# Kernel tuning notes

Measured on AMD Instinct MI355X. Metric: run time of the kernel, lower is better.

The kernel has to match this reference:

```python
import jax, jax.numpy as jnp
import numpy as np

K = 5        # up_kernel
SIG = 2      # scale_factor
PAD = K // 2

def _conv(x, w, b, pad):
    y = jax.lax.conv_general_dilated(
        x, w, window_strides=(1, 1), padding=[(pad, pad), (pad, pad)],
        dimension_numbers=('NCHW', 'OIHW', 'NCHW'))
    return y + b[None, :, None, None]

def setup_inputs() -> dict:
    key = jax.random.key(0)
    k1, k2, k3 = jax.random.split(key, 3)
    n, c, h, w = 4, 256, 64, 64
    comp_c = 64
    enc_out = K * K * 1 * SIG * SIG  # 100
    x = jax.random.normal(k1, (n, c, h, w), dtype=jnp.float32)
    w_comp = jax.random.normal(k2, (comp_c, c, 1, 1), dtype=jnp.float32) * (1.0 / np.sqrt(c))
    b_comp = jnp.zeros((comp_c,), dtype=jnp.float32)
    w_enc = jax.random.normal(k3, (enc_out, comp_c, 3, 3), dtype=jnp.float32) * 0.001
    b_enc = jnp.zeros((enc_out,), dtype=jnp.float32)
    return {"x": x, "w_comp": w_comp, "b_comp": b_comp, "w_enc": w_enc, "b_enc": b_enc}

def reference(x, w_comp, b_comp, w_enc, b_enc):
    n, c, h, w = x.shape
    # 1) channel compressor (1x1 conv) + content encoder (3x3 conv, pad 1)
    compressed = _conv(x, w_comp, b_comp, pad=0)
    mask = _conv(compressed, w_enc, b_enc, pad=1)        # [n, K*K*SIG*SIG, h, w]
    # 2) kernel_normalizer: pixel_shuffle(sigma) then softmax over K*K
    # torch pixel_shuffle channel layout: (K*K, SIG, SIG)
    mask = mask.reshape(n, K * K, SIG, SIG, h, w)
    mask = jax.nn.softmax(mask, axis=1)                   # softmax over kernel taps
    # 3) CARAFE reassembly: gather KxK window around each low-res source pixel
    xp = jnp.pad(x, ((0, 0), (0, 0), (PAD, PAD), (PAD, PAD)))
    # patches: [n, c, K*K, h, w]  (zero-padded borders)
    patches = jnp.stack(
        [xp[:, :, di:di + h, dj:dj + w] for di in range(K) for dj in range(K)],
        axis=2)
    # out[n,c,h*SIG+i, w*SIG+j] = sum_k patches[n,c,k,h,w] * mask[n,k,i,j,h,w]
    out = jnp.einsum('nkijhw,nckhw->nchiwj', mask, patches)
    return out.reshape(n, c, h * SIG, w * SIG)
```

## Files before the change

kernel.cpp:

```cpp
#include <hip/hip_runtime.h>

#define HW      4096
#define W_DIM   64
#define C_IN    256
#define NK      25
#define NQ      112

typedef __bf16 bf16x4 __attribute__((ext_vector_type(4)));
typedef __bf16 bf16x8 __attribute__((ext_vector_type(8)));
typedef float  f32x4  __attribute__((ext_vector_type(4)));
typedef float  f32x2  __attribute__((ext_vector_type(2)));

static __device__ __forceinline__ unsigned short f2bf(float f) {
    unsigned x = __float_as_uint(f);
    return (unsigned short)((x + 0x7fffu + ((x >> 16) & 1u)) >> 16);
}
static __device__ __forceinline__ float bflo2f(unsigned u) { return __uint_as_float(u << 16); }
static __device__ __forceinline__ float bfhi2f(unsigned u) { return __uint_as_float(u & 0xffff0000u); }

__global__ __launch_bounds__(256) void k_prep(const float* __restrict__ wenc,
                                              const float* __restrict__ wcomp,
                                              unsigned short* __restrict__ wtb,
                                              unsigned short* __restrict__ wct) {
    int idx = blockIdx.x * 256 + threadIdx.x;
    if (idx < 64512) {
        int c = idx & 63;
        int t2 = idx >> 6;
        int kq = t2 % NQ;
        int tap = t2 / NQ;
        float v = (kq < 100) ? wenc[(kq * 64 + c) * 9 + tap] : 0.0f;
        wtb[idx] = f2bf(v);
    } else if (idx < 80896) {
        int j = idx - 64512;
        wct[j] = f2bf(wcomp[j]);
    }
}

__global__ __launch_bounds__(256) void k_compress(const float* __restrict__ x,
        const unsigned short* __restrict__ wct, const float* __restrict__ bcomp,
        unsigned short* __restrict__ comp) {
    __shared__ unsigned short As[64 * 260];
    __shared__ unsigned short Bs[64 * 260];
    __shared__ float sbc[64];
    int n = blockIdx.y, p0 = blockIdx.x * 64;
    int tid = threadIdx.x, wv = tid >> 6, lane = tid & 63;
    int l15 = lane & 15, l4 = lane >> 4;
    if (tid < 64) sbc[tid] = bcomp[tid];

    const float* xp = x + (size_t)n * C_IN * HW + p0;
#pragma unroll
    for (int s = 0; s < 32; ++s) {
        int cp = s * 4 + wv;
        float a = xp[(size_t)(2 * cp) * HW + lane];
        float b = xp[(size_t)(2 * cp + 1) * HW + lane];
        unsigned pk = (unsigned)f2bf(a) | ((unsigned)f2bf(b) << 16);
        *(unsigned*)(As + lane * 260 + cp * 2) = pk;
    }
    const unsigned* wsrc = (const unsigned*)wct;
#pragma unroll
    for (int s = 0; s < 32; ++s) {
        int slot = s * 256 + tid;
        int cc = slot >> 7, c2 = slot & 127;
        *(unsigned*)(Bs + cc * 260 + c2 * 2) = wsrc[cc * 128 + c2];
    }
    __syncthreads();

    f32x4 acc[4];
#pragma unroll
    for (int nt = 0; nt < 4; ++nt) acc[nt] = (f32x4){0.f, 0.f, 0.f, 0.f};
#pragma unroll
    for (int ck = 0; ck < 8; ++ck) {
        int ko = ck * 32 + l4 * 8;
        bf16x4 alo = *(const bf16x4*)(As + (wv * 16 + l15) * 260 + ko);
        bf16x4 ahi = *(const bf16x4*)(As + (wv * 16 + l15) * 260 + ko + 4);
        bf16x8 af = __builtin_shufflevector(alo, ahi, 0, 1, 2, 3, 4, 5, 6, 7);
#pragma unroll
        for (int nt = 0; nt < 4; ++nt) {
            bf16x4 blo = *(const bf16x4*)(Bs + (nt * 16 + l15) * 260 + ko);
            bf16x4 bhi = *(const bf16x4*)(Bs + (nt * 16 + l15) * 260 + ko + 4);
            bf16x8 bfr = __builtin_shufflevector(blo, bhi, 0, 1, 2, 3, 4, 5, 6, 7);
            acc[nt] = __builtin_amdgcn_mfma_f32_16x16x32_bf16(af, bfr, acc[nt], 0, 0, 0);
        }
    }
    unsigned short* op = comp + ((size_t)n * HW + p0 + wv * 16 + l4 * 4) * 64;
#pragma unroll
    for (int reg = 0; reg < 4; ++reg)
#pragma unroll
        for (int nt = 0; nt < 4; ++nt) {
            int cc = nt * 16 + l15;
            op[(size_t)reg * 64 + cc] = f2bf(acc[nt][reg] + sbc[cc]);
        }
}

#define CREC    136
#define SB0     13600
#define BSTRIDE 15232
#define EPI_PAD 116
__global__ __launch_bounds__(256) void k_enc(
        const unsigned short* __restrict__ comp,
        const unsigned short* __restrict__ wtb,
        const float* __restrict__ benc,
        unsigned short* __restrict__ mask) {
    __shared__ __align__(16) unsigned char smem[SB0 + 2 * BSTRIDE];
    __shared__ float sbias[NQ];
    int n = blockIdx.y, tile = blockIdx.x;
    int h0 = (tile >> 3) * 8, w0 = (tile & 7) * 8;
    int tid = threadIdx.x, wv = tid >> 6, lane = tid & 63;
    int l15 = lane & 15, l4 = lane >> 4;
    if (tid < NQ) sbias[tid] = (tid < 100) ? benc[tid] : 0.0f;

    const uint4* csrc = (const uint4*)(comp + (size_t)n * HW * 64);
#pragma unroll
    for (int pass = 0; pass < 4; ++pass) {
        int s = pass * 256 + tid;
        if (s < 800) {
            int px = s >> 3, j = s & 7;
            int gh = h0 + px / 10 - 1, gw = w0 + px % 10 - 1;
            uint4 v = make_uint4(0u, 0u, 0u, 0u);
            if ((unsigned)gh < 64u && (unsigned)gw < 64u)
                v = csrc[(size_t)(gh * 64 + gw) * 8 + j];
            *(uint2*)(smem + px * CREC + j * 16)     = make_uint2(v.x, v.y);
            *(uint2*)(smem + px * CREC + j * 16 + 8) = make_uint2(v.z, v.w);
        }
    }
    {
        const uint4* bs = (const uint4*)wtb;
#pragma unroll
        for (int pass = 0; pass < 4; ++pass) {
            int s = pass * 256 + tid;
            if (s < 896) {
                uint4 v = bs[s];
                int kq = s >> 3, j = s & 7;
                *(uint2*)(smem + SB0 + kq * CREC + j * 16)     = make_uint2(v.x, v.y);
                *(uint2*)(smem + SB0 + kq * CREC + j * 16 + 8) = make_uint2(v.z, v.w);
            }
        }
    }
    uint4 pre[4];
    {
        const uint4* bs = (const uint4*)(wtb + (size_t)1 * NQ * 64);
#pragma unroll
        for (int pass = 0; pass < 4; ++pass) {
            int s = pass * 256 + tid;
            if (s < 896) pre[pass] = bs[s];
        }
    }

    f32x4 acc[7];
#pragma unroll
    for (int nt = 0; nt < 7; ++nt) acc[nt] = (f32x4){0.f, 0.f, 0.f, 0.f};
    int r_t = 2 * wv + (l15 >> 3), cl = l15 & 7;

    for (int tap = 0; tap < 9; ++tap) {
        __syncthreads();
        if (tap < 8) {
            unsigned char* nbuf = smem + SB0 + ((tap + 1) & 1) * BSTRIDE;
#pragma unroll
            for (int pass = 0; pass < 4; ++pass) {
                int s = pass * 256 + tid;
                if (s < 896) {
                    int kq = s >> 3, j = s & 7;
                    *(uint2*)(nbuf + kq * CREC + j * 16)     = make_uint2(pre[pass].x, pre[pass].y);
                    *(uint2*)(nbuf + kq * CREC + j * 16 + 8) = make_uint2(pre[pass].z, pre[pass].w);
                }
            }
            if (tap < 7) {
                const uint4* bs = (const uint4*)(wtb + (size_t)(tap + 2) * NQ * 64);
#pragma unroll
                for (int pass = 0; pass < 4; ++pass) {
                    int s = pass * 256 + tid;
                    if (s < 896) pre[pass] = bs[s];
                }
            }
        }
        int ti = tap / 3, tj = tap % 3;
        int apx = (r_t + ti) * 10 + cl + tj;
        const unsigned char* cbuf = smem + SB0 + (tap & 1) * BSTRIDE;
#pragma unroll
        for (int ck = 0; ck < 2; ++ck) {
            int ko = ck * 64 + l4 * 16;
            bf16x4 alo = *(const bf16x4*)(smem + apx * CREC + ko);
            bf16x4 ahi = *(const bf16x4*)(smem + apx * CREC + ko + 8);
            bf16x8 af = __builtin_shufflevector(alo, ahi, 0, 1, 2, 3, 4, 5, 6, 7);
#pragma unroll
            for (int nt = 0; nt < 7; ++nt) {
                bf16x4 blo = *(const bf16x4*)(cbuf + (nt * 16 + l15) * CREC + ko);
                bf16x4 bhi = *(const bf16x4*)(cbuf + (nt * 16 + l15) * CREC + ko + 8);
                bf16x8 bfr = __builtin_shufflevector(blo, bhi, 0, 1, 2, 3, 4, 5, 6, 7);
                acc[nt] = __builtin_amdgcn_mfma_f32_16x16x32_bf16(af, bfr, acc[nt], 0, 0, 0);
            }
        }
    }
    __syncthreads();

    float* smE = (float*)(smem + SB0) + (size_t)wv * 16 * EPI_PAD;
    unsigned short* maskn = mask + (size_t)n * HW * 100;
#pragma unroll
    for (int nt = 0; nt < 7; ++nt) {
        f32x4 v = acc[nt];
#pragma unroll
        for (int reg = 0; reg < 4; ++reg)
            smE[(l4 * 4 + reg) * EPI_PAD + nt * 16 + l15] = v[reg];
    }
    {
        int spx = lane >> 2, q = lane & 3;
        float* row = smE + spx * EPI_PAD;
        float v[NK], mx = -1e30f;
#pragma unroll
        for (int k = 0; k < NK; ++k) {
            v[k] = row[4 * k + q] + sbias[4 * k + q];
            mx = fmaxf(mx, v[k]);
        }
        float ssum = 0.f;
#pragma unroll
        for (int k = 0; k < NK; ++k) { v[k] = __expf(v[k] - mx); ssum += v[k]; }
        float inv = 1.0f / ssum;
#pragma unroll
        for (int k = 0; k < NK; ++k) row[4 * k + q] = v[k] * inv;
    }
#pragma unroll
    for (int i = 0; i < 7; ++i) {
        int idx = i * 64 + lane;
        if (idx < 400) {
            int spx = idx / 25, f4 = idx % 25;
            int rr = 2 * wv + (spx >> 3), cc2 = spx & 7;
            size_t p = (size_t)(h0 + rr) * 64 + (w0 + cc2);
            const float* sp = smE + spx * EPI_PAD + f4 * 4;
            unsigned u0 = (unsigned)f2bf(sp[0]) | ((unsigned)f2bf(sp[1]) << 16);
            unsigned u1 = (unsigned)f2bf(sp[2]) | ((unsigned)f2bf(sp[3]) << 16);
            *(uint2*)(maskn + p * 100 + f4 * 4) = make_uint2(u0, u1);
        }
    }
}

#define XSTR2 20
#define MSTR2 108
__global__ __launch_bounds__(256, 6) void k_reassemble(const float* __restrict__ x,
        const unsigned short* __restrict__ mask, float* __restrict__ out) {
    __shared__ __align__(16) float xs[144 * XSTR2];
    __shared__ __align__(16) unsigned short ms[64 * MSTR2];
    int flat = blockIdx.x;
    int nf = (flat & 7) * 512 + (flat >> 3);
    int tile = nf & 63, cg = (nf >> 6) & 15, n = nf >> 10;
    int h0 = (tile >> 3) * 8, w0 = (tile & 7) * 8;
    int tid = threadIdx.x;

    const float* xb = x + ((size_t)n * C_IN + cg * 16) * HW;
#pragma unroll
    for (int i = 0; i < 5; ++i) {
        int s = i * 256 + tid;
        if (s < 1152) {
            int c = s / 72, rem = s % 72;
            int r = rem / 6, j = rem % 6;
            int gh = h0 - 2 + r, gw = w0 - 2 + j * 2;
            float2 v = make_float2(0.f, 0.f);
            if ((unsigned)gh < 64u && (unsigned)gw < 64u)
                v = *(const float2*)(xb + (size_t)c * HW + gh * W_DIM + gw);
            int px = r * 12 + j * 2;
            xs[px * XSTR2 + c]       = v.x;
            xs[(px + 1) * XSTR2 + c] = v.y;
        }
    }
    const unsigned short* mp = mask + (size_t)n * HW * 100;
#pragma unroll
    for (int i = 0; i < 7; ++i) {
        int s = i * 256 + tid;
        if (s < 1600) {
            int px = s / 25, q = s % 25;
            int gp = (h0 + (px >> 3)) * W_DIM + w0 + (px & 7);
            *(uint2*)(ms + px * MSTR2 + q * 4) =
                *(const uint2*)(mp + (size_t)gp * 100 + q * 4);
        }
    }
    __syncthreads();

    int px = tid & 63, w = tid >> 6;
    int wx = px & 7, hy = px >> 3;
    f32x4 acc0 = {0.f, 0.f, 0.f, 0.f}, acc1 = {0.f, 0.f, 0.f, 0.f};
    f32x4 acc2 = {0.f, 0.f, 0.f, 0.f}, acc3 = {0.f, 0.f, 0.f, 0.f};
    const unsigned short* mrow = ms + px * MSTR2;
#pragma unroll
    for (int di = 0; di < 5; ++di)
#pragma unroll
        for (int dj = 0; dj < 5; ++dj) {
            int t = di * 5 + dj;
            uint2 mw = *(const uint2*)(mrow + t * 4);
            f32x4 xv = *(const f32x4*)(xs + ((hy + di) * 12 + wx + dj) * XSTR2 + w * 4);
            acc0 += xv * bflo2f(mw.x);
            acc1 += xv * bfhi2f(mw.x);
            acc2 += xv * bflo2f(mw.y);
            acc3 += xv * bfhi2f(mw.y);
        }
#pragma unroll
    for (int u = 0; u < 4; ++u) {
        float* ob = out + (((size_t)n * C_IN + cg * 16 + w * 4 + u) * 128 + 2 * (h0 + hy)) * 128
                        + 2 * (w0 + wx);
        *(float2*)(ob)       = make_float2(acc0[u], acc1[u]);
        *(float2*)(ob + 128) = make_float2(acc2[u], acc3[u]);
    }
}

extern "C" void kernel_launch(void* const* d_in, const int* in_sizes, int n_in,
                              void* d_out, int out_size, void* d_ws, size_t ws_size,
                              hipStream_t stream) {
    const float* x      = (const float*)d_in[0];
    const float* w_comp = (const float*)d_in[1];
    const float* b_comp = (const float*)d_in[2];
    const float* w_enc  = (const float*)d_in[3];
    const float* b_enc  = (const float*)d_in[4];
    float* out = (float*)d_out;
    unsigned char* ws = (unsigned char*)d_ws;

    unsigned short* comp  = (unsigned short*)(ws);
    unsigned short* wtb   = (unsigned short*)(ws + 2097152);
    unsigned short* wct   = (unsigned short*)(ws + 2226176);
    unsigned short* maskp = (unsigned short*)(ws + 2258944);

    hipLaunchKernelGGL(k_prep,       dim3(316),      dim3(256), 0, stream,
                       w_enc, w_comp, wtb, wct);
    hipLaunchKernelGGL(k_compress,   dim3(64, 4),    dim3(256), 0, stream,
                       x, wct, b_comp, comp);
    hipLaunchKernelGGL(k_enc,        dim3(64, 4),    dim3(256), 0, stream,
                       comp, wtb, b_enc, maskp);
    hipLaunchKernelGGL(k_reassemble, dim3(4096),     dim3(256), 0, stream,
                       x, maskp, out);
}
```

Measured before the change: 121.3 us.

## Spread compress and encoder GEMMs over more waves and smaller tiles

The compress kernel now runs 1024 threads per block, so each of the 16 waves computes one 16x16 output tile instead of four waves each computing four. The encoder kernel halves its spatial tile to 4x8 pixels and doubles the grid. Its four waves split the seven output-channel tiles between two row groups, and the softmax and store epilogue now runs on a shared block-wide staging buffer. The aim is more parallelism and occupancy on small grids (256 blocks) to hide latency. The cost is more barriers, a larger halo overhead, and redundant weight staging per block.

```diff
diff --git a/kernel.cpp b/kernel.cpp
--- a/kernel.cpp
+++ b/kernel.cpp
@@ -36,7 +36,7 @@
     }
 }
 
-__global__ __launch_bounds__(256) void k_compress(const float* __restrict__ x,
+__global__ __launch_bounds__(1024) void k_compress(const float* __restrict__ x,
         const unsigned short* __restrict__ wct, const float* __restrict__ bcomp,
         unsigned short* __restrict__ comp) {
     __shared__ unsigned short As[64 * 260];
@@ -49,8 +49,8 @@
 
     const float* xp = x + (size_t)n * C_IN * HW + p0;
 #pragma unroll
-    for (int s = 0; s < 32; ++s) {
-        int cp = s * 4 + wv;
+    for (int s = 0; s < 8; ++s) {
+        int cp = s * 16 + wv;
         float a = xp[(size_t)(2 * cp) * HW + lane];
         float b = xp[(size_t)(2 * cp + 1) * HW + lane];
         unsigned pk = (unsigned)f2bf(a) | ((unsigned)f2bf(b) << 16);
@@ -58,42 +58,36 @@
     }
     const unsigned* wsrc = (const unsigned*)wct;
 #pragma unroll
-    for (int s = 0; s < 32; ++s) {
-        int slot = s * 256 + tid;
+    for (int s = 0; s < 8; ++s) {
+        int slot = s * 1024 + tid;
         int cc = slot >> 7, c2 = slot & 127;
         *(unsigned*)(Bs + cc * 260 + c2 * 2) = wsrc[cc * 128 + c2];
     }
     __syncthreads();
 
-    f32x4 acc[4];
-#pragma unroll
-    for (int nt = 0; nt < 4; ++nt) acc[nt] = (f32x4){0.f, 0.f, 0.f, 0.f};
+    int mt = wv >> 2, nt = wv & 3;
+    f32x4 acc = (f32x4){0.f, 0.f, 0.f, 0.f};
 #pragma unroll
     for (int ck = 0; ck < 8; ++ck) {
         int ko = ck * 32 + l4 * 8;
-        bf16x4 alo = *(const bf16x4*)(As + (wv * 16 + l15) * 260 + ko);
-        bf16x4 ahi = *(const bf16x4*)(As + (wv * 16 + l15) * 260 + ko + 4);
+        bf16x4 alo = *(const bf16x4*)(As + (mt * 16 + l15) * 260 + ko);
+        bf16x4 ahi = *(const bf16x4*)(As + (mt * 16 + l15) * 260 + ko + 4);
         bf16x8 af = __builtin_shufflevector(alo, ahi, 0, 1, 2, 3, 4, 5, 6, 7);
-#pragma unroll
-        for (int nt = 0; nt < 4; ++nt) {
-            bf16x4 blo = *(const bf16x4*)(Bs + (nt * 16 + l15) * 260 + ko);
-            bf16x4 bhi = *(const bf16x4*)(Bs + (nt * 16 + l15) * 260 + ko + 4);
-            bf16x8 bfr = __builtin_shufflevector(blo, bhi, 0, 1, 2, 3, 4, 5, 6, 7);
-            acc[nt] = __builtin_amdgcn_mfma_f32_16x16x32_bf16(af, bfr, acc[nt], 0, 0, 0);
-        }
-    }
-    unsigned short* op = comp + ((size_t)n * HW + p0 + wv * 16 + l4 * 4) * 64;
-#pragma unroll
-    for (int reg = 0; reg < 4; ++reg)
-#pragma unroll
-        for (int nt = 0; nt < 4; ++nt) {
-            int cc = nt * 16 + l15;
-            op[(size_t)reg * 64 + cc] = f2bf(acc[nt][reg] + sbc[cc]);
-        }
+        bf16x4 blo = *(const bf16x4*)(Bs + (nt * 16 + l15) * 260 + ko);
+        bf16x4 bhi = *(const bf16x4*)(Bs + (nt * 16 + l15) * 260 + ko + 4);
+        bf16x8 bfr = __builtin_shufflevector(blo, bhi, 0, 1, 2, 3, 4, 5, 6, 7);
+        acc = __builtin_amdgcn_mfma_f32_16x16x32_bf16(af, bfr, acc, 0, 0, 0);
+    }
+    unsigned short* op = comp + ((size_t)n * HW + p0 + mt * 16 + l4 * 4) * 64 + nt * 16;
+#pragma unroll
+    for (int reg = 0; reg < 4; ++reg) {
+        int cc = nt * 16 + l15;
+        op[(size_t)reg * 64 + l15] = f2bf(acc[reg] + sbc[cc]);
+    }
 }
 
 #define CREC    136
-#define SB0     13600
+#define SB0E    8160
 #define BSTRIDE 15232
 #define EPI_PAD 116
 __global__ __launch_bounds__(256) void k_enc(
@@ -101,19 +95,19 @@
         const unsigned short* __restrict__ wtb,
         const float* __restrict__ benc,
         unsigned short* __restrict__ mask) {
-    __shared__ __align__(16) unsigned char smem[SB0 + 2 * BSTRIDE];
+    __shared__ __align__(16) unsigned char smem[SB0E + 2 * BSTRIDE];
     __shared__ float sbias[NQ];
     int n = blockIdx.y, tile = blockIdx.x;
-    int h0 = (tile >> 3) * 8, w0 = (tile & 7) * 8;
+    int h0 = (tile >> 3) * 4, w0 = (tile & 7) * 8;
     int tid = threadIdx.x, wv = tid >> 6, lane = tid & 63;
     int l15 = lane & 15, l4 = lane >> 4;
     if (tid < NQ) sbias[tid] = (tid < 100) ? benc[tid] : 0.0f;
 
     const uint4* csrc = (const uint4*)(comp + (size_t)n * HW * 64);
 #pragma unroll
-    for (int pass = 0; pass < 4; ++pass) {
+    for (int pass = 0; pass < 2; ++pass) {
         int s = pass * 256 + tid;
-        if (s < 800) {
+        if (s < 480) {
             int px = s >> 3, j = s & 7;
             int gh = h0 + px / 10 - 1, gw = w0 + px % 10 - 1;
             uint4 v = make_uint4(0u, 0u, 0u, 0u);
@@ -131,8 +125,8 @@
             if (s < 896) {
                 uint4 v = bs[s];
                 int kq = s >> 3, j = s & 7;
-                *(uint2*)(smem + SB0 + kq * CREC + j * 16)     = make_uint2(v.x, v.y);
-                *(uint2*)(smem + SB0 + kq * CREC + j * 16 + 8) = make_uint2(v.z, v.w);
+                *(uint2*)(smem + SB0E + kq * CREC + j * 16)     = make_uint2(v.x, v.y);
+                *(uint2*)(smem + SB0E + kq * CREC + j * 16 + 8) = make_uint2(v.z, v.w);
             }
         }
     }
@@ -146,15 +140,16 @@
         }
     }
 
-    f32x4 acc[7];
-#pragma unroll
-    for (int nt = 0; nt < 7; ++nt) acc[nt] = (f32x4){0.f, 0.f, 0.f, 0.f};
-    int r_t = 2 * wv + (l15 >> 3), cl = l15 & 7;
+    f32x4 acc[4];
+#pragma unroll
+    for (int k = 0; k < 4; ++k) acc[k] = (f32x4){0.f, 0.f, 0.f, 0.f};
+    int mt = wv & 1, ng = wv >> 1;
+    int r_t = 2 * mt + (l15 >> 3), cl = l15 & 7;
 
     for (int tap = 0; tap < 9; ++tap) {
         __syncthreads();
         if (tap < 8) {
-            unsigned char* nbuf = smem + SB0 + ((tap + 1) & 1) * BSTRIDE;
+            unsigned char* nbuf = smem + SB0E + ((tap + 1) & 1) * BSTRIDE;
 #pragma unroll
             for (int pass = 0; pass < 4; ++pass) {
                 int s = pass * 256 + tid;
@@ -175,7 +170,7 @@
         }
         int ti = tap / 3, tj = tap % 3;
         int apx = (r_t + ti) * 10 + cl + tj;
-        const unsigned char* cbuf = smem + SB0 + (tap & 1) * BSTRIDE;
+        const unsigned char* cbuf = smem + SB0E + (tap & 1) * BSTRIDE;
 #pragma unroll
         for (int ck = 0; ck < 2; ++ck) {
             int ko = ck * 64 + l4 * 16;
@@ -183,27 +178,34 @@
             bf16x4 ahi = *(const bf16x4*)(smem + apx * CREC + ko + 8);
             bf16x8 af = __builtin_shufflevector(alo, ahi, 0, 1, 2, 3, 4, 5, 6, 7);
 #pragma unroll
-            for (int nt = 0; nt < 7; ++nt) {
-                bf16x4 blo = *(const bf16x4*)(cbuf + (nt * 16 + l15) * CREC + ko);
-                bf16x4 bhi = *(const bf16x4*)(cbuf + (nt * 16 + l15) * CREC + ko + 8);
-                bf16x8 bfr = __builtin_shufflevector(blo, bhi, 0, 1, 2, 3, 4, 5, 6, 7);
-                acc[nt] = __builtin_amdgcn_mfma_f32_16x16x32_bf16(af, bfr, acc[nt], 0, 0, 0);
+            for (int k = 0; k < 4; ++k) {
+                int nt = ng + 2 * k;
+                if (nt < 7) {
+                    bf16x4 blo = *(const bf16x4*)(cbuf + (nt * 16 + l15) * CREC + ko);
+                    bf16x4 bhi = *(const bf16x4*)(cbuf + (nt * 16 + l15) * CREC + ko + 8);
+                    bf16x8 bfr = __builtin_shufflevector(blo, bhi, 0, 1, 2, 3, 4, 5, 6, 7);
+                    acc[k] = __builtin_amdgcn_mfma_f32_16x16x32_bf16(af, bfr, acc[k], 0, 0, 0);
+                }
             }
         }
     }
     __syncthreads();
 
-    float* smE = (float*)(smem + SB0) + (size_t)wv * 16 * EPI_PAD;
+    float* smE = (float*)(smem + SB0E);
     unsigned short* maskn = mask + (size_t)n * HW * 100;
 #pragma unroll
-    for (int nt = 0; nt < 7; ++nt) {
-        f32x4 v = acc[nt];
-#pragma unroll
-        for (int reg = 0; reg < 4; ++reg)
-            smE[(l4 * 4 + reg) * EPI_PAD + nt * 16 + l15] = v[reg];
-    }
-    {
-        int spx = lane >> 2, q = lane & 3;
+    for (int k = 0; k < 4; ++k) {
+        int nt = ng + 2 * k;
+        if (nt < 7) {
+            f32x4 v = acc[k];
+#pragma unroll
+            for (int reg = 0; reg < 4; ++reg)
+                smE[(mt * 16 + l4 * 4 + reg) * EPI_PAD + nt * 16 + l15] = v[reg];
+        }
+    }
+    __syncthreads();
+    if (tid < 128) {
+        int spx = tid >> 2, q = tid & 3;
         float* row = smE + spx * EPI_PAD;
         float v[NK], mx = -1e30f;
 #pragma unroll
@@ -218,12 +220,13 @@
 #pragma unroll
         for (int k = 0; k < NK; ++k) row[4 * k + q] = v[k] * inv;
     }
-#pragma unroll
-    for (int i = 0; i < 7; ++i) {
-        int idx = i * 64 + lane;
-        if (idx < 400) {
+    __syncthreads();
+#pragma unroll
+    for (int i = 0; i < 4; ++i) {
+        int idx = i * 256 + tid;
+        if (idx < 800) {
             int spx = idx / 25, f4 = idx % 25;
-            int rr = 2 * wv + (spx >> 3), cc2 = spx & 7;
+            int rr = spx >> 3, cc2 = spx & 7;
             size_t p = (size_t)(h0 + rr) * 64 + (w0 + cc2);
             const float* sp = smE + spx * EPI_PAD + f4 * 4;
             unsigned u0 = (unsigned)f2bf(sp[0]) | ((unsigned)f2bf(sp[1]) << 16);
@@ -316,12 +319,12 @@
     unsigned short* wct   = (unsigned short*)(ws + 2226176);
     unsigned short* maskp = (unsigned short*)(ws + 2258944);
 
-    hipLaunchKernelGGL(k_prep,       dim3(316),      dim3(256), 0, stream,
+    hipLaunchKernelGGL(k_prep,       dim3(316),      dim3(256),  0, stream,
                        w_enc, w_comp, wtb, wct);
-    hipLaunchKernelGGL(k_compress,   dim3(64, 4),    dim3(256), 0, stream,
+    hipLaunchKernelGGL(k_compress,   dim3(64, 4),    dim3(1024), 0, stream,
                        x, wct, b_comp, comp);
-    hipLaunchKernelGGL(k_enc,        dim3(64, 4),    dim3(256), 0, stream,
+    hipLaunchKernelGGL(k_enc,        dim3(128, 4),   dim3(256),  0, stream,
                        comp, wtb, b_enc, maskp);
-    hipLaunchKernelGGL(k_reassemble, dim3(4096),     dim3(256), 0, stream,
+    hipLaunchKernelGGL(k_reassemble, dim3(4096),     dim3(256),  0, stream,
                        x, maskp, out);
 }
```

Measured after the change: 128.6 us. 1.06x slower.

## Double threads per block in compress and encoder kernels, splitting MFMA N tiles across waves

Applied to the files above, without the earlier changes.

Both the 1x1 compressor GEMM and the 3x3 encoder GEMM now launch 512 threads per block. Each wave computes a subset of the output column tiles instead of all of them, so more waves per block share the same shared-memory staging. With only 256 blocks per launch, the aim is more latency hiding and higher occupancy. The encoder epilogue becomes block-wide with extra barriers, and only half of the threads run the softmax.

```diff
diff --git a/kernel.cpp b/kernel.cpp
--- a/kernel.cpp
+++ b/kernel.cpp
@@ -36,7 +36,7 @@
     }
 }
 
-__global__ __launch_bounds__(256) void k_compress(const float* __restrict__ x,
+__global__ __launch_bounds__(512) void k_compress(const float* __restrict__ x,
         const unsigned short* __restrict__ wct, const float* __restrict__ bcomp,
         unsigned short* __restrict__ comp) {
     __shared__ unsigned short As[64 * 260];
@@ -49,8 +49,8 @@
 
     const float* xp = x + (size_t)n * C_IN * HW + p0;
 #pragma unroll
-    for (int s = 0; s < 32; ++s) {
-        int cp = s * 4 + wv;
+    for (int s = 0; s < 16; ++s) {
+        int cp = s * 8 + wv;
         float a = xp[(size_t)(2 * cp) * HW + lane];
         float b = xp[(size_t)(2 * cp + 1) * HW + lane];
         unsigned pk = (unsigned)f2bf(a) | ((unsigned)f2bf(b) << 16);
@@ -58,37 +58,39 @@
     }
     const unsigned* wsrc = (const unsigned*)wct;
 #pragma unroll
-    for (int s = 0; s < 32; ++s) {
-        int slot = s * 256 + tid;
+    for (int s = 0; s < 16; ++s) {
+        int slot = s * 512 + tid;
         int cc = slot >> 7, c2 = slot & 127;
         *(unsigned*)(Bs + cc * 260 + c2 * 2) = wsrc[cc * 128 + c2];
     }
     __syncthreads();
 
-    f32x4 acc[4];
-#pragma unroll
-    for (int nt = 0; nt < 4; ++nt) acc[nt] = (f32x4){0.f, 0.f, 0.f, 0.f};
+    int mt = wv >> 1, nb = (wv & 1) * 2;
+    f32x4 acc[2];
+#pragma unroll
+    for (int j = 0; j < 2; ++j) acc[j] = (f32x4){0.f, 0.f, 0.f, 0.f};
 #pragma unroll
     for (int ck = 0; ck < 8; ++ck) {
         int ko = ck * 32 + l4 * 8;
-        bf16x4 alo = *(const bf16x4*)(As + (wv * 16 + l15) * 260 + ko);
-        bf16x4 ahi = *(const bf16x4*)(As + (wv * 16 + l15) * 260 + ko + 4);
+        bf16x4 alo = *(const bf16x4*)(As + (mt * 16 + l15) * 260 + ko);
+        bf16x4 ahi = *(const bf16x4*)(As + (mt * 16 + l15) * 260 + ko + 4);
         bf16x8 af = __builtin_shufflevector(alo, ahi, 0, 1, 2, 3, 4, 5, 6, 7);
 #pragma unroll
-        for (int nt = 0; nt < 4; ++nt) {
+        for (int j = 0; j < 2; ++j) {
+            int nt = nb + j;
             bf16x4 blo = *(const bf16x4*)(Bs + (nt * 16 + l15) * 260 + ko);
             bf16x4 bhi = *(const bf16x4*)(Bs + (nt * 16 + l15) * 260 + ko + 4);
             bf16x8 bfr = __builtin_shufflevector(blo, bhi, 0, 1, 2, 3, 4, 5, 6, 7);
-            acc[nt] = __builtin_amdgcn_mfma_f32_16x16x32_bf16(af, bfr, acc[nt], 0, 0, 0);
-        }
-    }
-    unsigned short* op = comp + ((size_t)n * HW + p0 + wv * 16 + l4 * 4) * 64;
+            acc[j] = __builtin_amdgcn_mfma_f32_16x16x32_bf16(af, bfr, acc[j], 0, 0, 0);
+        }
+    }
+    unsigned short* op = comp + ((size_t)n * HW + p0 + mt * 16 + l4 * 4) * 64;
 #pragma unroll
     for (int reg = 0; reg < 4; ++reg)
 #pragma unroll
-        for (int nt = 0; nt < 4; ++nt) {
-            int cc = nt * 16 + l15;
-            op[(size_t)reg * 64 + cc] = f2bf(acc[nt][reg] + sbc[cc]);
+        for (int j = 0; j < 2; ++j) {
+            int cc = (nb + j) * 16 + l15;
+            op[(size_t)reg * 64 + cc] = f2bf(acc[j][reg] + sbc[cc]);
         }
 }
 
@@ -96,7 +98,7 @@
 #define SB0     13600
 #define BSTRIDE 15232
 #define EPI_PAD 116
-__global__ __launch_bounds__(256) void k_enc(
+__global__ __launch_bounds__(512) void k_enc(
         const unsigned short* __restrict__ comp,
         const unsigned short* __restrict__ wtb,
         const float* __restrict__ benc,
@@ -111,8 +113,8 @@
 
     const uint4* csrc = (const uint4*)(comp + (size_t)n * HW * 64);
 #pragma unroll
-    for (int pass = 0; pass < 4; ++pass) {
-        int s = pass * 256 + tid;
+    for (int pass = 0; pass < 2; ++pass) {
+        int s = pass * 512 + tid;
         if (s < 800) {
             int px = s >> 3, j = s & 7;
             int gh = h0 + px / 10 - 1, gw = w0 + px % 10 - 1;
@@ -126,8 +128,8 @@
     {
         const uint4* bs = (const uint4*)wtb;
 #pragma unroll
-        for (int pass = 0; pass < 4; ++pass) {
-            int s = pass * 256 + tid;
+        for (int pass = 0; pass < 2; ++pass) {
+            int s = pass * 512 + tid;
             if (s < 896) {
                 uint4 v = bs[s];
                 int kq = s >> 3, j = s & 7;
@@ -136,28 +138,29 @@
             }
         }
     }
-    uint4 pre[4];
+    uint4 pre[2];
     {
         const uint4* bs = (const uint4*)(wtb + (size_t)1 * NQ * 64);
 #pragma unroll
-        for (int pass = 0; pass < 4; ++pass) {
-            int s = pass * 256 + tid;
+        for (int pass = 0; pass < 2; ++pass) {
+            int s = pass * 512 + tid;
             if (s < 896) pre[pass] = bs[s];
         }
     }
 
-    f32x4 acc[7];
-#pragma unroll
-    for (int nt = 0; nt < 7; ++nt) acc[nt] = (f32x4){0.f, 0.f, 0.f, 0.f};
-    int r_t = 2 * wv + (l15 >> 3), cl = l15 & 7;
+    f32x4 acc[4];
+#pragma unroll
+    for (int k = 0; k < 4; ++k) acc[k] = (f32x4){0.f, 0.f, 0.f, 0.f};
+    int mq = wv & 3, g = wv >> 2;
+    int r_t = 2 * mq + (l15 >> 3), cl = l15 & 7;
 
     for (int tap = 0; tap < 9; ++tap) {
         __syncthreads();
         if (tap < 8) {
             unsigned char* nbuf = smem + SB0 + ((tap + 1) & 1) * BSTRIDE;
 #pragma unroll
-            for (int pass = 0; pass < 4; ++pass) {
-                int s = pass * 256 + tid;
+            for (int pass = 0; pass < 2; ++pass) {
+                int s = pass * 512 + tid;
                 if (s < 896) {
                     int kq = s >> 3, j = s & 7;
                     *(uint2*)(nbuf + kq * CREC + j * 16)     = make_uint2(pre[pass].x, pre[pass].y);
@@ -167,8 +170,8 @@
             if (tap < 7) {
                 const uint4* bs = (const uint4*)(wtb + (size_t)(tap + 2) * NQ * 64);
 #pragma unroll
-                for (int pass = 0; pass < 4; ++pass) {
-                    int s = pass * 256 + tid;
+                for (int pass = 0; pass < 2; ++pass) {
+                    int s = pass * 512 + tid;
                     if (s < 896) pre[pass] = bs[s];
                 }
             }
@@ -183,28 +186,35 @@
             bf16x4 ahi = *(const bf16x4*)(smem + apx * CREC + ko + 8);
             bf16x8 af = __builtin_shufflevector(alo, ahi, 0, 1, 2, 3, 4, 5, 6, 7);
 #pragma unroll
-            for (int nt = 0; nt < 7; ++nt) {
-                bf16x4 blo = *(const bf16x4*)(cbuf + (nt * 16 + l15) * CREC + ko);
-                bf16x4 bhi = *(const bf16x4*)(cbuf + (nt * 16 + l15) * CREC + ko + 8);
-                bf16x8 bfr = __builtin_shufflevector(blo, bhi, 0, 1, 2, 3, 4, 5, 6, 7);
-                acc[nt] = __builtin_amdgcn_mfma_f32_16x16x32_bf16(af, bfr, acc[nt], 0, 0, 0);
+            for (int k = 0; k < 4; ++k) {
+                int nt = g * 4 + k;
+                if (nt < 7) {
+                    bf16x4 blo = *(const bf16x4*)(cbuf + (nt * 16 + l15) * CREC + ko);
+                    bf16x4 bhi = *(const bf16x4*)(cbuf + (nt * 16 + l15) * CREC + ko + 8);
+                    bf16x8 bfr = __builtin_shufflevector(blo, bhi, 0, 1, 2, 3, 4, 5, 6, 7);
+                    acc[k] = __builtin_amdgcn_mfma_f32_16x16x32_bf16(af, bfr, acc[k], 0, 0, 0);
+                }
             }
         }
     }
     __syncthreads();
 
-    float* smE = (float*)(smem + SB0) + (size_t)wv * 16 * EPI_PAD;
+    float* smE = (float*)(smem + SB0);
     unsigned short* maskn = mask + (size_t)n * HW * 100;
 #pragma unroll
-    for (int nt = 0; nt < 7; ++nt) {
-        f32x4 v = acc[nt];
-#pragma unroll
-        for (int reg = 0; reg < 4; ++reg)
-            smE[(l4 * 4 + reg) * EPI_PAD + nt * 16 + l15] = v[reg];
-    }
-    {
-        int spx = lane >> 2, q = lane & 3;
-        float* row = smE + spx * EPI_PAD;
+    for (int k = 0; k < 4; ++k) {
+        int nt = g * 4 + k;
+        if (nt < 7) {
+            f32x4 v = acc[k];
+#pragma unroll
+            for (int reg = 0; reg < 4; ++reg)
+                smE[(mq * 16 + l4 * 4 + reg) * EPI_PAD + nt * 16 + l15] = v[reg];
+        }
+    }
+    __syncthreads();
+    if (tid < 256) {
+        int r = tid >> 2, q = tid & 3;
+        float* row = smE + r * EPI_PAD;
         float v[NK], mx = -1e30f;
 #pragma unroll
         for (int k = 0; k < NK; ++k) {
@@ -218,14 +228,15 @@
 #pragma unroll
         for (int k = 0; k < NK; ++k) row[4 * k + q] = v[k] * inv;
     }
-#pragma unroll
-    for (int i = 0; i < 7; ++i) {
-        int idx = i * 64 + lane;
-        if (idx < 400) {
-            int spx = idx / 25, f4 = idx % 25;
-            int rr = 2 * wv + (spx >> 3), cc2 = spx & 7;
+    __syncthreads();
+#pragma unroll
+    for (int i = 0; i < 4; ++i) {
+        int idx = i * 512 + tid;
+        if (idx < 1600) {
+            int r = idx / 25, f4 = idx % 25;
+            int rr = 2 * (r >> 4) + ((r >> 3) & 1), cc2 = r & 7;
             size_t p = (size_t)(h0 + rr) * 64 + (w0 + cc2);
-            const float* sp = smE + spx * EPI_PAD + f4 * 4;
+            const float* sp = smE + r * EPI_PAD + f4 * 4;
             unsigned u0 = (unsigned)f2bf(sp[0]) | ((unsigned)f2bf(sp[1]) << 16);
             unsigned u1 = (unsigned)f2bf(sp[2]) | ((unsigned)f2bf(sp[3]) << 16);
             *(uint2*)(maskn + p * 100 + f4 * 4) = make_uint2(u0, u1);
@@ -318,9 +329,9 @@
 
     hipLaunchKernelGGL(k_prep,       dim3(316),      dim3(256), 0, stream,
                        w_enc, w_comp, wtb, wct);
-    hipLaunchKernelGGL(k_compress,   dim3(64, 4),    dim3(256), 0, stream,
+    hipLaunchKernelGGL(k_compress,   dim3(64, 4),    dim3(512), 0, stream,
                        x, wct, b_comp, comp);
-    hipLaunchKernelGGL(k_enc,        dim3(64, 4),    dim3(256), 0, stream,
+    hipLaunchKernelGGL(k_enc,        dim3(64, 4),    dim3(512), 0, stream,
                        comp, wtb, b_enc, maskp);
     hipLaunchKernelGGL(k_reassemble, dim3(4096),     dim3(256), 0, stream,
                        x, maskp, out);
```

Result: slower. 125.3 us (+3.3%).

## Fold weight prep into compress kernel and read mask directly in reassembly

Applied to the files above, without the earlier changes.

Removes the separate k_prep launch. The 1x1 compressor weights are now converted to bf16 inline while they are loaded into shared memory, and the encoder-weight transpose runs in extra blocks appended to the compress grid. The reassembly kernel no longer stages mask rows in LDS; each thread loads its own 5 mask quads per row straight from global memory. This trades one launch and one LDS staging pass for redundant per-thread global mask reads, since all four waves read the same mask row, and for uncoalesced strided loads.

```diff
diff --git a/kernel.cpp b/kernel.cpp
--- a/kernel.cpp
+++ b/kernel.cpp
@@ -18,32 +18,27 @@
 static __device__ __forceinline__ float bflo2f(unsigned u) { return __uint_as_float(u << 16); }
 static __device__ __forceinline__ float bfhi2f(unsigned u) { return __uint_as_float(u & 0xffff0000u); }
 
-__global__ __launch_bounds__(256) void k_prep(const float* __restrict__ wenc,
-                                              const float* __restrict__ wcomp,
-                                              unsigned short* __restrict__ wtb,
-                                              unsigned short* __restrict__ wct) {
-    int idx = blockIdx.x * 256 + threadIdx.x;
-    if (idx < 64512) {
+__global__ __launch_bounds__(256) void k_compress(const float* __restrict__ x,
+        const float* __restrict__ wcomp, const float* __restrict__ bcomp,
+        const float* __restrict__ wenc,
+        unsigned short* __restrict__ comp, unsigned short* __restrict__ wtb) {
+    __shared__ unsigned short As[64 * 260];
+    __shared__ unsigned short Bs[64 * 260];
+    __shared__ float sbc[64];
+    int b = blockIdx.x;
+    int tid = threadIdx.x;
+    if (b >= 256) {
+        int idx = (b - 256) * 256 + tid;
         int c = idx & 63;
         int t2 = idx >> 6;
         int kq = t2 % NQ;
         int tap = t2 / NQ;
         float v = (kq < 100) ? wenc[(kq * 64 + c) * 9 + tap] : 0.0f;
         wtb[idx] = f2bf(v);
-    } else if (idx < 80896) {
-        int j = idx - 64512;
-        wct[j] = f2bf(wcomp[j]);
-    }
-}
-
-__global__ __launch_bounds__(256) void k_compress(const float* __restrict__ x,
-        const unsigned short* __restrict__ wct, const float* __restrict__ bcomp,
-        unsigned short* __restrict__ comp) {
-    __shared__ unsigned short As[64 * 260];
-    __shared__ unsigned short Bs[64 * 260];
-    __shared__ float sbc[64];
-    int n = blockIdx.y, p0 = blockIdx.x * 64;
-    int tid = threadIdx.x, wv = tid >> 6, lane = tid & 63;
+        return;
+    }
+    int n = b >> 6, p0 = (b & 63) * 64;
+    int wv = tid >> 6, lane = tid & 63;
     int l15 = lane & 15, l4 = lane >> 4;
     if (tid < 64) sbc[tid] = bcomp[tid];
 
@@ -52,16 +47,18 @@
     for (int s = 0; s < 32; ++s) {
         int cp = s * 4 + wv;
         float a = xp[(size_t)(2 * cp) * HW + lane];
-        float b = xp[(size_t)(2 * cp + 1) * HW + lane];
-        unsigned pk = (unsigned)f2bf(a) | ((unsigned)f2bf(b) << 16);
+        float bb = xp[(size_t)(2 * cp + 1) * HW + lane];
+        unsigned pk = (unsigned)f2bf(a) | ((unsigned)f2bf(bb) << 16);
         *(unsigned*)(As + lane * 260 + cp * 2) = pk;
     }
-    const unsigned* wsrc = (const unsigned*)wct;
+    const float2* wf = (const float2*)wcomp;
 #pragma unroll
     for (int s = 0; s < 32; ++s) {
         int slot = s * 256 + tid;
         int cc = slot >> 7, c2 = slot & 127;
-        *(unsigned*)(Bs + cc * 260 + c2 * 2) = wsrc[cc * 128 + c2];
+        float2 v = wf[cc * 128 + c2];
+        unsigned pk = (unsigned)f2bf(v.x) | ((unsigned)f2bf(v.y) << 16);
+        *(unsigned*)(Bs + cc * 260 + c2 * 2) = pk;
     }
     __syncthreads();
 
@@ -234,11 +231,9 @@
 }
 
 #define XSTR2 20
-#define MSTR2 108
 __global__ __launch_bounds__(256, 6) void k_reassemble(const float* __restrict__ x,
         const unsigned short* __restrict__ mask, float* __restrict__ out) {
     __shared__ __align__(16) float xs[144 * XSTR2];
-    __shared__ __align__(16) unsigned short ms[64 * MSTR2];
     int flat = blockIdx.x;
     int nf = (flat & 7) * 512 + (flat >> 3);
     int tile = nf & 63, cg = (nf >> 6) & 15, n = nf >> 10;
@@ -261,36 +256,32 @@
             xs[(px + 1) * XSTR2 + c] = v.y;
         }
     }
-    const unsigned short* mp = mask + (size_t)n * HW * 100;
-#pragma unroll
-    for (int i = 0; i < 7; ++i) {
-        int s = i * 256 + tid;
-        if (s < 1600) {
-            int px = s / 25, q = s % 25;
-            int gp = (h0 + (px >> 3)) * W_DIM + w0 + (px & 7);
-            *(uint2*)(ms + px * MSTR2 + q * 4) =
-                *(const uint2*)(mp + (size_t)gp * 100 + q * 4);
-        }
-    }
     __syncthreads();
 
     int px = tid & 63, w = tid >> 6;
     int wx = px & 7, hy = px >> 3;
+    const unsigned short* mrow = mask + (size_t)n * HW * 100
+                               + (size_t)((h0 + hy) * W_DIM + (w0 + wx)) * 100;
     f32x4 acc0 = {0.f, 0.f, 0.f, 0.f}, acc1 = {0.f, 0.f, 0.f, 0.f};
     f32x4 acc2 = {0.f, 0.f, 0.f, 0.f}, acc3 = {0.f, 0.f, 0.f, 0.f};
-    const unsigned short* mrow = ms + px * MSTR2;
-#pragma unroll
-    for (int di = 0; di < 5; ++di)
+#pragma unroll
+    for (int di = 0; di < 5; ++di) {
+        uint2 mq0 = *(const uint2*)(mrow + (di * 5 + 0) * 4);
+        uint2 mq1 = *(const uint2*)(mrow + (di * 5 + 1) * 4);
+        uint2 mq2 = *(const uint2*)(mrow + (di * 5 + 2) * 4);
+        uint2 mq3 = *(const uint2*)(mrow + (di * 5 + 3) * 4);
+        uint2 mq4 = *(const uint2*)(mrow + (di * 5 + 4) * 4);
 #pragma unroll
         for (int dj = 0; dj < 5; ++dj) {
-            int t = di * 5 + dj;
-            uint2 mw = *(const uint2*)(mrow + t * 4);
+            uint2 mw = (dj == 0) ? mq0 : (dj == 1) ? mq1 : (dj == 2) ? mq2
+                     : (dj == 3) ? mq3 : mq4;
             f32x4 xv = *(const f32x4*)(xs + ((hy + di) * 12 + wx + dj) * XSTR2 + w * 4);
             acc0 += xv * bflo2f(mw.x);
             acc1 += xv * bfhi2f(mw.x);
             acc2 += xv * bflo2f(mw.y);
             acc3 += xv * bfhi2f(mw.y);
         }
+    }
 #pragma unroll
     for (int u = 0; u < 4; ++u) {
         float* ob = out + (((size_t)n * C_IN + cg * 16 + w * 4 + u) * 128 + 2 * (h0 + hy)) * 128
@@ -313,13 +304,10 @@
 
     unsigned short* comp  = (unsigned short*)(ws);
     unsigned short* wtb   = (unsigned short*)(ws + 2097152);
-    unsigned short* wct   = (unsigned short*)(ws + 2226176);
-    unsigned short* maskp = (unsigned short*)(ws + 2258944);
-
-    hipLaunchKernelGGL(k_prep,       dim3(316),      dim3(256), 0, stream,
-                       w_enc, w_comp, wtb, wct);
-    hipLaunchKernelGGL(k_compress,   dim3(64, 4),    dim3(256), 0, stream,
-                       x, wct, b_comp, comp);
+    unsigned short* maskp = (unsigned short*)(ws + 2226176);
+
+    hipLaunchKernelGGL(k_compress,   dim3(508),      dim3(256), 0, stream,
+                       x, w_comp, b_comp, w_enc, comp, wtb);
     hipLaunchKernelGGL(k_enc,        dim3(64, 4),    dim3(256), 0, stream,
                        comp, wtb, b_enc, maskp);
     hipLaunchKernelGGL(k_reassemble, dim3(4096),     dim3(256), 0, stream,
```

New measurement: 120.6 us, median of 2. About the same (-0.6%).
